# Kernel optimization log

Hardware: AMD Instinct MI355X
Metric: run time of the kernel (lower is better)

## Reference

```python
import jax, jax.numpy as jnp
import numpy as np

HEADS = 8
LATENT_LEN = 64
SEQ_LEN = 8192
DIM = 512
DIM_HEAD = DIM // HEADS
LN_EPS = 1e-5


def setup_inputs() -> dict:
    key = jax.random.key(0)
    k1, k2, k3 = jax.random.split(key, 3)
    b, n = 16, SEQ_LEN + LATENT_LEN
    x = jax.random.normal(k1, (b, n, DIM), dtype=jnp.float32)
    # torch nn.Linear weights are [out_features, in_features]
    wq = jax.random.normal(k2, (DIM, DIM), dtype=jnp.float32) * (DIM ** -0.5)
    wkv = jax.random.normal(k3, (DIM, DIM), dtype=jnp.float32) * (DIM ** -0.5)
    ln_g = jnp.ones((DIM_HEAD,), dtype=jnp.float32)
    ln_b = jnp.zeros((DIM_HEAD,), dtype=jnp.float32)
    return {"x": x, "wq": wq, "wkv": wkv, "ln_g": ln_g, "ln_b": ln_b}


def _rotate_half(t):
    # lucidrains-style rotate_half: split last dim in two halves, (-x2, x1)
    d2 = t.shape[-1] // 2
    t1, t2 = t[..., :d2], t[..., d2:]
    return jnp.concatenate([-t2, t1], axis=-1)


def _rotary_emb(n, d, dtype):
    inv_freq = 1.0 / (10000.0 ** (jnp.arange(0, d, 2, dtype=jnp.float32) / d))
    freqs = jnp.arange(n, dtype=jnp.float32)[:, None] * inv_freq[None, :]  # [n, d/2]
    emb = jnp.concatenate([freqs, freqs], axis=-1)  # [n, d]
    return jnp.cos(emb).astype(dtype), jnp.sin(emb).astype(dtype)


def reference(x, wq, wkv, ln_g, ln_b):
    b, n, dim = x.shape
    h, d = HEADS, DIM_HEAD
    context_len = n - LATENT_LEN
    scale = d ** -0.5

    q = x @ wq.T   # [b, n, dim]
    kv = x @ wkv.T # [b, n, dim]
    # rearrange 'b n (h d) -> (b h) n d'
    to_bh = lambda t: t.reshape(b, n, h, d).transpose(0, 2, 1, 3).reshape(b * h, n, d)
    q, kv = to_bh(q), to_bh(kv)

    cos, sin = _rotary_emb(n, d, x.dtype)  # [n, d] broadcast over (b h)
    rope = lambda t: t * cos + _rotate_half(t) * sin
    q, kv = rope(q), rope(kv)

    q = q * scale
    q_latent = q[:, context_len:, :]  # [(b h), latent, d]

    # LayerNorm over head dim applied to V (kv)
    mu = jnp.mean(kv, axis=-1, keepdims=True)
    var = jnp.mean(jnp.square(kv - mu), axis=-1, keepdims=True)
    lkv = (kv - mu) * jax.lax.rsqrt(var + LN_EPS) * ln_g + ln_b

    sim = jnp.einsum('bid,bjd->bij', q_latent, kv)  # [(b h), latent, n]
    attn = jax.nn.softmax(sim, axis=-1)
    out = jnp.einsum('bij,bjd->bid', attn, lkv)     # [(b h), latent, d]

    # rearrange '(b h) n d -> b n (h d)'
    out = out.reshape(b, h, LATENT_LEN, d).transpose(0, 2, 1, 3).reshape(b, LATENT_LEN, dim)
    return out
```

## Files before the change

kernel.cpp:

```cpp
#include <hip/hip_runtime.h>
#include <hip/hip_bf16.h>
#include <math.h>

#define SEQ_LEN 8192
#define LAT 64
#define NPOS 8256
#define NBATCH 16
#define NHEADS 8
#define DH 64
#define DIM 512
#define NBH 128
#define NROWS 132096
#define NCHUNK 4
#define NTILES 129

typedef unsigned short u16;
typedef unsigned int   u32;
using short8 = __attribute__((ext_vector_type(8))) short;
using f32x4  = __attribute__((ext_vector_type(4))) float;

static __device__ __forceinline__ float bf2f(u16 u) {
  union { u32 i; float f; } v; v.i = ((u32)u) << 16; return v.f;
}
static __device__ __forceinline__ u16 f2bf(float f) {
  union { float f; u32 i; } v; v.f = f;
  u32 x = v.i;
  return (u16)((x + 0x7fffu + ((x >> 16) & 1u)) >> 16);
}
static __device__ __forceinline__ void gload_lds16(const void* g, void* l) {
  __builtin_amdgcn_global_load_lds(
      (const __attribute__((address_space(1))) unsigned int*)g,
      (__attribute__((address_space(3))) unsigned int*)l, 16, 0, 0);
}

__global__ void k_rtable(float* __restrict__ ctab, float* __restrict__ stab) {
  int idx = blockIdx.x * 256 + threadIdx.x;
  int pos = idx >> 5, i = idx & 31;
  float inv = (float)(1.0 / pow(10000.0, (double)(2 * i) / 64.0));
  float ang = (float)pos * inv;
  ctab[idx] = cosf(ang);
  stab[idx] = sinf(ang);
}

__global__ __launch_bounds__(256) void k_wcast(const float* __restrict__ wkv, u16* __restrict__ wbf) {
  size_t i = (size_t)blockIdx.x * 256 + threadIdx.x;
  const float4* src = (const float4*)wkv;
  float4 a = src[2 * i], b = src[2 * i + 1];
  uint4 o;
  o.x = (u32)f2bf(a.x) | ((u32)f2bf(a.y) << 16);
  o.y = (u32)f2bf(a.z) | ((u32)f2bf(a.w) << 16);
  o.z = (u32)f2bf(b.x) | ((u32)f2bf(b.y) << 16);
  o.w = (u32)f2bf(b.z) | ((u32)f2bf(b.w) << 16);
  ((uint4*)wbf)[i] = o;
}

__global__ __launch_bounds__(256) void k_qproj(
    const float* __restrict__ x, const float* __restrict__ wq,
    const float* __restrict__ ctab, const float* __restrict__ stab,
    u16* __restrict__ qws) {
  __shared__ __align__(16) float xs[8 * 512];
  int t = threadIdx.x;
  int lr0 = blockIdx.x * 8;
  int batch = lr0 >> 6;
  int lat0 = lr0 & 63;
  for (int u = 0; u < 4; ++u) {
    int e = u * 256 + t;
    int row = e >> 7, c4 = e & 127;
    size_t m = (size_t)batch * NPOS + SEQ_LEN + lat0 + row;
    ((float4*)xs)[e] = ((const float4*)(x + m * DIM))[c4];
  }
  __syncthreads();
  float acc0[8], acc1[8];
#pragma unroll
  for (int r = 0; r < 8; ++r) { acc0[r] = 0.f; acc1[r] = 0.f; }
  const float4* w0 = (const float4*)(wq + (size_t)t * DIM);
  const float4* w1 = (const float4*)(wq + (size_t)(t + 256) * DIM);
  for (int kk = 0; kk < 128; ++kk) {
    float4 a = w0[kk], b = w1[kk];
#pragma unroll
    for (int r = 0; r < 8; ++r) {
      float4 xv = ((const float4*)xs)[r * 128 + kk];
      acc0[r] = fmaf(a.x, xv.x, fmaf(a.y, xv.y, fmaf(a.z, xv.z, fmaf(a.w, xv.w, acc0[r]))));
      acc1[r] = fmaf(b.x, xv.x, fmaf(b.y, xv.y, fmaf(b.z, xv.z, fmaf(b.w, xv.w, acc1[r]))));
    }
  }
  __syncthreads();
#pragma unroll
  for (int r = 0; r < 8; ++r) { xs[r * 512 + t] = acc0[r]; xs[r * 512 + t + 256] = acc1[r]; }
  __syncthreads();
  int rh = t >> 2, sub = t & 3;
  int row = rh >> 3, head = rh & 7;
  int lat = lat0 + row, pos = SEQ_LEN + lat;
  int bh = batch * 8 + head;
  u16* qd = qws + ((size_t)bh * LAT + lat) * DH;
#pragma unroll
  for (int u = 0; u < 8; ++u) {
    int i = sub * 8 + u;
    float v1 = xs[row * 512 + head * 64 + i];
    float v2 = xs[row * 512 + head * 64 + i + 32];
    float cc = ctab[pos * 32 + i], ss = stab[pos * 32 + i];
    qd[i]      = f2bf((v1 * cc - v2 * ss) * 0.125f);
    qd[i + 32] = f2bf((v2 * cc + v1 * ss) * 0.125f);
  }
}

__global__ __launch_bounds__(256, 2) void k_kvgemm(
    const float* __restrict__ x, const u16* __restrict__ wbf,
    const float* __restrict__ ctab, const float* __restrict__ stab,
    u16* __restrict__ kvws, float2* __restrict__ stats) {
  __shared__ __align__(16) char smem[65536];
  float* Cs = (float*)smem;
  int t = threadIdx.x;
  int lane = t & 63, w = t >> 6;
  int wr = w >> 1, wc = w & 1;
  int c = lane & 15, g = lane >> 4;
  int s = (blockIdx.x & 7) * 516 + (blockIdx.x >> 3);
  int n0 = (s & 3) * 128;
  size_t m0 = (size_t)(s >> 2) * 128;

  f32x4 acc[4][4];
#pragma unroll
  for (int mt = 0; mt < 4; ++mt)
#pragma unroll
    for (int nt = 0; nt < 4; ++nt) acc[mt][nt] = (f32x4){0.f, 0.f, 0.f, 0.f};

  int ar = t >> 3, ac8 = t & 7;
  const float* axbase = x + (m0 + ar) * DIM + ac8 * 8;
  int aswz = (ac8 * 16) ^ ((ar & 7) << 4);
  int tcs = ((t & 7) ^ (ar & 7)) << 4;
  const char* bgsrc = (const char*)(wbf + (size_t)(n0 + ar) * DIM) + tcs;

  float4 a0[4], a1[4];
  auto issueA = [&](int kt) {
#pragma unroll
    for (int u = 0; u < 4; ++u) {
      const float* p = axbase + (size_t)u * 32 * DIM + kt * 64;
      a0[u] = *(const float4*)p;
      a1[u] = *(const float4*)(p + 4);
    }
  };
  auto issueB = [&](int kt, char* bbuf) {
    const char* bg = bgsrc + kt * 128;
    char* bl = bbuf + t * 16;
#pragma unroll
    for (int u = 0; u < 4; ++u) gload_lds16(bg + (size_t)u * 32 * 1024, bl + u * 4096);
  };
  auto writeA = [&](char* abuf) {
#pragma unroll
    for (int u = 0; u < 4; ++u) {
      short8 o;
      o[0] = (short)f2bf(a0[u].x); o[1] = (short)f2bf(a0[u].y);
      o[2] = (short)f2bf(a0[u].z); o[3] = (short)f2bf(a0[u].w);
      o[4] = (short)f2bf(a1[u].x); o[5] = (short)f2bf(a1[u].y);
      o[6] = (short)f2bf(a1[u].z); o[7] = (short)f2bf(a1[u].w);
      *(short8*)(abuf + (u * 32 + ar) * 128 + aswz) = o;
    }
  };

  issueA(0);
  issueB(0, smem + 32768);
  writeA(smem);
  __syncthreads();

#pragma unroll
  for (int kt = 0; kt < 8; ++kt) {
    char* Acur = smem + (kt & 1) * 16384;
    char* Bcur = smem + 32768 + (kt & 1) * 16384;
    char* Anxt = smem + ((kt & 1) ^ 1) * 16384;
    char* Bnxt = smem + 32768 + ((kt & 1) ^ 1) * 16384;
    if (kt < 7) { issueA(kt + 1); issueB(kt + 1, Bnxt); }
#pragma unroll
    for (int ks = 0; ks < 2; ++ks) {
      short8 am[4], bn[4];
#pragma unroll
      for (int mt = 0; mt < 4; ++mt) {
        int row = wr * 64 + mt * 16 + c;
        am[mt] = *(const short8*)(Acur + row * 128 + ((ks * 64 + g * 16) ^ ((row & 7) << 4)));
      }
#pragma unroll
      for (int nt = 0; nt < 4; ++nt) {
        int row = wc * 64 + nt * 16 + c;
        bn[nt] = *(const short8*)(Bcur + row * 128 + ((ks * 64 + g * 16) ^ ((row & 7) << 4)));
      }
#pragma unroll
      for (int mt = 0; mt < 4; ++mt)
#pragma unroll
        for (int nt = 0; nt < 4; ++nt)
          acc[mt][nt] = __builtin_amdgcn_mfma_f32_16x16x32_bf16(am[mt], bn[nt], acc[mt][nt], 0, 0, 0);
    }
    if (kt < 7) writeA(Anxt);
    __syncthreads();
  }

  for (int p = 0; p < 2; ++p) {
    __syncthreads();
    if (wr == p) {
#pragma unroll
      for (int mt = 0; mt < 4; ++mt)
#pragma unroll
        for (int nt = 0; nt < 4; ++nt)
#pragma unroll
          for (int r = 0; r < 4; ++r)
            Cs[(mt * 16 + 4 * g + r) * 132 + wc * 64 + nt * 16 + c] = acc[mt][nt][r];
    }
    __syncthreads();
    if (t < 128) {
      int r_ = t & 63, hh = t >> 6;
      float v[64];
      const float4* crow = (const float4*)(Cs + r_ * 132 + hh * 64);
#pragma unroll
      for (int q = 0; q < 16; ++q) {
        float4 f = crow[q];
        v[4 * q] = f.x; v[4 * q + 1] = f.y; v[4 * q + 2] = f.z; v[4 * q + 3] = f.w;
      }
      int mi = (int)(m0 + p * 64 + r_);
      int b = mi / NPOS, pos = mi % NPOS;
      const float* ct = ctab + pos * 32;
      const float* st = stab + pos * 32;
#pragma unroll
      for (int i = 0; i < 32; ++i) {
        float cc = ct[i], ss = st[i];
        float v1 = v[i], v2 = v[i + 32];
        v[i]      = v1 * cc - v2 * ss;
        v[i + 32] = v2 * cc + v1 * ss;
      }
      float sum = 0.f;
#pragma unroll
      for (int e = 0; e < 64; ++e) sum += v[e];
      float mu = sum * 0.015625f;
      float sq = 0.f;
#pragma unroll
      for (int e = 0; e < 64; ++e) { float d = v[e] - mu; sq = fmaf(d, d, sq); }
      float rstd = rsqrtf(sq * 0.015625f + 1e-5f);
      int head = (n0 >> 6) + hh;
      int bh = b * 8 + head;
      u32 pk[32];
#pragma unroll
      for (int e = 0; e < 32; ++e) pk[e] = (u32)f2bf(v[2 * e]) | ((u32)f2bf(v[2 * e + 1]) << 16);
      uint4* dst = (uint4*)(kvws + ((size_t)bh * NPOS + pos) * DH);
#pragma unroll
      for (int u = 0; u < 8; ++u) dst[u] = make_uint4(pk[4 * u], pk[4 * u + 1], pk[4 * u + 2], pk[4 * u + 3]);
      stats[(size_t)bh * NPOS + pos] = make_float2(mu, rstd);
    }
  }
}

__global__ __launch_bounds__(256) void k_attn(
    const u16* __restrict__ qws, const u16* __restrict__ kvws,
    const float2* __restrict__ stats, const float* __restrict__ lng, const float* __restrict__ lnb,
    float* __restrict__ pout, float* __restrict__ pml) {
  __shared__ __align__(16) u16 LT[64 * 64];
  __shared__ __align__(16) u16 Pl[4][16 * 64];
  __shared__ float gl[64], bl[64];
  int t = threadIdx.x;
  int lane = t & 63, w = t >> 6;
  int c = lane & 15, g = lane >> 4;
  int bh = blockIdx.y, chunk = blockIdx.x;
  int tt0 = chunk * 33;
  int tt1 = tt0 + 33; if (tt1 > NTILES) tt1 = NTILES;
  if (t < 64) { gl[t] = lng[t]; bl[t] = lnb[t]; }
  short8 qa[2];
  {
    const u16* qrow = qws + ((size_t)bh * LAT + w * 16 + c) * DH;
    qa[0] = *(const short8*)(qrow + 8 * g);
    qa[1] = *(const short8*)(qrow + 32 + 8 * g);
  }
  f32x4 oacc[4];
#pragma unroll
  for (int nt = 0; nt < 4; ++nt) oacc[nt] = (f32x4){0.f, 0.f, 0.f, 0.f};
  float m_run[4], l_run[4];
#pragma unroll
  for (int r = 0; r < 4; ++r) { m_run[r] = -INFINITY; l_run[r] = 0.f; }
  int sj = t & 63, sw = t >> 6;
  for (int tt = tt0; tt < tt1; ++tt) {
    int j0 = tt * 64;
    __syncthreads();
    {
      const u16* src = kvws + ((size_t)bh * NPOS + j0 + sj) * DH + 16 * sw;
      short8 v0 = *(const short8*)src;
      short8 v1 = *(const short8*)(src + 8);
      float2 stv = stats[(size_t)bh * NPOS + j0 + sj];
      float A = stv.y, C = -stv.x * stv.y;
      char* ltb = (char*)LT;
#pragma unroll
      for (int e = 0; e < 16; ++e) {
        int dd = 16 * sw + e;
        u16 uv = (u16)((e < 8) ? v0[e] : v1[e - 8]);
        float y = fmaf(bf2f(uv), A, C);
        y = fmaf(y, gl[dd], bl[dd]);
        *(u16*)(ltb + dd * 128 + ((2 * sj) ^ ((dd & 7) << 4))) = f2bf(y);
      }
    }
    __syncthreads();
    f32x4 sacc[4];
#pragma unroll
    for (int jn = 0; jn < 4; ++jn) sacc[jn] = (f32x4){0.f, 0.f, 0.f, 0.f};
    const u16* kb = kvws + ((size_t)bh * NPOS + j0) * DH;
#pragma unroll
    for (int ks = 0; ks < 2; ++ks)
#pragma unroll
      for (int jn = 0; jn < 4; ++jn) {
        short8 kf = *(const short8*)(kb + (size_t)(jn * 16 + c) * DH + ks * 32 + 8 * g);
        sacc[jn] = __builtin_amdgcn_mfma_f32_16x16x32_bf16(qa[ks], kf, sacc[jn], 0, 0, 0);
      }
    char* pb = (char*)Pl[w];
#pragma unroll
    for (int r = 0; r < 4; ++r) {
      float mt0 = fmaxf(fmaxf(sacc[0][r], sacc[1][r]), fmaxf(sacc[2][r], sacc[3][r]));
      mt0 = fmaxf(mt0, __shfl_xor(mt0, 1));
      mt0 = fmaxf(mt0, __shfl_xor(mt0, 2));
      mt0 = fmaxf(mt0, __shfl_xor(mt0, 4));
      mt0 = fmaxf(mt0, __shfl_xor(mt0, 8));
      float mnew = fmaxf(m_run[r], mt0);
      float corr = __expf(m_run[r] - mnew);
      m_run[r] = mnew;
      float ts = 0.f;
#pragma unroll
      for (int jn = 0; jn < 4; ++jn) {
        float p = __expf(sacc[jn][r] - mnew);
        sacc[jn][r] = p;
        ts += p;
      }
      ts += __shfl_xor(ts, 1); ts += __shfl_xor(ts, 2);
      ts += __shfl_xor(ts, 4); ts += __shfl_xor(ts, 8);
      l_run[r] = l_run[r] * corr + ts;
#pragma unroll
      for (int nt = 0; nt < 4; ++nt) oacc[nt][r] *= corr;
      int i = 4 * g + r;
      int isw = (i & 7) << 4;
#pragma unroll
      for (int jn = 0; jn < 4; ++jn) {
        int j = jn * 16 + c;
        *(u16*)(pb + i * 128 + ((2 * j) ^ isw)) = f2bf(sacc[jn][r]);
      }
    }
#pragma unroll
    for (int ks = 0; ks < 2; ++ks) {
      short8 pa = *(const short8*)(pb + c * 128 + ((ks * 64 + 16 * g) ^ ((c & 7) << 4)));
#pragma unroll
      for (int nt = 0; nt < 4; ++nt) {
        int dd = nt * 16 + c;
        short8 lv = *(const short8*)((char*)LT + dd * 128 + ((ks * 64 + 16 * g) ^ ((dd & 7) << 4)));
        oacc[nt] = __builtin_amdgcn_mfma_f32_16x16x32_bf16(pa, lv, oacc[nt], 0, 0, 0);
      }
    }
  }
  size_t ob = (size_t)bh * NCHUNK + chunk;
#pragma unroll
  for (int nt = 0; nt < 4; ++nt)
#pragma unroll
    for (int r = 0; r < 4; ++r) {
      int i = w * 16 + 4 * g + r;
      pout[(ob * 64 + i) * 64 + nt * 16 + c] = oacc[nt][r];
    }
  if (c == 0) {
#pragma unroll
    for (int r = 0; r < 4; ++r) {
      int i = w * 16 + 4 * g + r;
      pml[(ob * 2 + 0) * 64 + i] = m_run[r];
      pml[(ob * 2 + 1) * 64 + i] = l_run[r];
    }
  }
}

__global__ __launch_bounds__(256) void k_combine(
    const float* __restrict__ pout, const float* __restrict__ pml, float* __restrict__ out) {
  int bh = blockIdx.x, t = threadIdx.x;
  int i = t >> 2, dq = t & 3;
  float mv[NCHUNK], lv[NCHUNK];
#pragma unroll
  for (int cc = 0; cc < NCHUNK; ++cc) {
    size_t ob = (size_t)bh * NCHUNK + cc;
    mv[cc] = pml[(ob * 2 + 0) * 64 + i];
    lv[cc] = pml[(ob * 2 + 1) * 64 + i];
  }
  float M = fmaxf(fmaxf(mv[0], mv[1]), fmaxf(mv[2], mv[3]));
  float wsum = 0.f, wcf[NCHUNK];
#pragma unroll
  for (int cc = 0; cc < NCHUNK; ++cc) { wcf[cc] = __expf(mv[cc] - M); wsum = fmaf(wcf[cc], lv[cc], wsum); }
  float inv = 1.0f / wsum;
#pragma unroll
  for (int e = 0; e < 16; ++e) {
    int dd = dq * 16 + e;
    float a = 0.f;
#pragma unroll
    for (int cc = 0; cc < NCHUNK; ++cc)
      a = fmaf(wcf[cc], pout[(((size_t)bh * NCHUNK + cc) * 64 + i) * 64 + dd], a);
    out[((size_t)(bh >> 3) * LAT + i) * DIM + (bh & 7) * DH + dd] = a * inv;
  }
}

extern "C" void kernel_launch(void* const* d_in, const int* in_sizes, int n_in,
                              void* d_out, int out_size, void* d_ws, size_t ws_size,
                              hipStream_t stream) {
  const float* x   = (const float*)d_in[0];
  const float* wq  = (const float*)d_in[1];
  const float* wkv = (const float*)d_in[2];
  const float* lng = (const float*)d_in[3];
  const float* lnb = (const float*)d_in[4];
  float* out = (float*)d_out;
  char* ws = (char*)d_ws;
  size_t off = 0;
  auto alloc = [&](size_t bytes) { char* p = ws + off; off += (bytes + 255) & ~(size_t)255; return p; };
  float*  ctab  = (float*)alloc((size_t)NPOS * 32 * 4);
  float*  stab  = (float*)alloc((size_t)NPOS * 32 * 4);
  u16*    qws   = (u16*)alloc((size_t)NBH * LAT * DH * 2);
  u16*    kvws  = (u16*)alloc((size_t)NBH * NPOS * DH * 2);
  float2* stats = (float2*)alloc((size_t)NBH * NPOS * 8);
  float*  pout  = (float*)alloc((size_t)NBH * NCHUNK * 64 * 64 * 4);
  float*  pml   = (float*)alloc((size_t)NBH * NCHUNK * 2 * 64 * 4);
  u16*    wbf   = (u16*)alloc((size_t)DIM * DIM * 2);
  (void)in_sizes; (void)n_in; (void)out_size; (void)ws_size;

  hipLaunchKernelGGL(k_rtable, dim3(NPOS * 32 / 256), dim3(256), 0, stream, ctab, stab);
  hipLaunchKernelGGL(k_wcast, dim3(DIM * DIM / 8 / 256), dim3(256), 0, stream, wkv, wbf);
  hipLaunchKernelGGL(k_qproj, dim3(128), dim3(256), 0, stream, x, wq, ctab, stab, qws);
  hipLaunchKernelGGL(k_kvgemm, dim3(4128), dim3(256), 0, stream, x, wbf, ctab, stab, kvws, stats);
  hipLaunchKernelGGL(k_attn, dim3(NCHUNK, NBH), dim3(256), 0, stream, qws, kvws, stats, lng, lnb, pout, pml);
  hipLaunchKernelGGL(k_combine, dim3(NBH), dim3(256), 0, stream, pout, pml, out);
}
```

Before: 393.5 us.

## Fold LayerNorm of V into softmax weights and double attention split-K chunks

The attention kernel no longer normalizes each V tile in shared memory. It scales the probabilities by each key's rstd, accumulates a running sum of p*mu*rstd, and applies gamma, beta and the mean correction in the combine step. This removes per-element LayerNorm arithmetic and the gamma/beta shared-memory lookups from the inner loop. The number of KV chunks per head also goes from 4 to 8, doubling the grid from 512 to 1024 blocks for better occupancy, at the cost of more partial outputs to write and combine. Precision changes slightly because V is now fed raw in bf16 and P*rstd is rounded to bf16.

```diff
diff --git a/kernel.cpp b/kernel.cpp
--- a/kernel.cpp
+++ b/kernel.cpp
@@ -11,8 +11,9 @@
 #define DIM 512
 #define NBH 128
 #define NROWS 132096
-#define NCHUNK 4
+#define NCHUNK 8
 #define NTILES 129
+#define TPC 17
 
 typedef unsigned short u16;
 typedef unsigned int   u32;
@@ -247,18 +248,16 @@
 
 __global__ __launch_bounds__(256) void k_attn(
     const u16* __restrict__ qws, const u16* __restrict__ kvws,
-    const float2* __restrict__ stats, const float* __restrict__ lng, const float* __restrict__ lnb,
+    const float2* __restrict__ stats,
     float* __restrict__ pout, float* __restrict__ pml) {
   __shared__ __align__(16) u16 LT[64 * 64];
   __shared__ __align__(16) u16 Pl[4][16 * 64];
-  __shared__ float gl[64], bl[64];
   int t = threadIdx.x;
   int lane = t & 63, w = t >> 6;
   int c = lane & 15, g = lane >> 4;
   int bh = blockIdx.y, chunk = blockIdx.x;
-  int tt0 = chunk * 33;
-  int tt1 = tt0 + 33; if (tt1 > NTILES) tt1 = NTILES;
-  if (t < 64) { gl[t] = lng[t]; bl[t] = lnb[t]; }
+  int tt0 = chunk * TPC;
+  int tt1 = tt0 + TPC; if (tt1 > NTILES) tt1 = NTILES;
   short8 qa[2];
   {
     const u16* qrow = qws + ((size_t)bh * LAT + w * 16 + c) * DH;
@@ -268,9 +267,9 @@
   f32x4 oacc[4];
 #pragma unroll
   for (int nt = 0; nt < 4; ++nt) oacc[nt] = (f32x4){0.f, 0.f, 0.f, 0.f};
-  float m_run[4], l_run[4];
-#pragma unroll
-  for (int r = 0; r < 4; ++r) { m_run[r] = -INFINITY; l_run[r] = 0.f; }
+  float m_run[4], l_run[4], q2_run[4];
+#pragma unroll
+  for (int r = 0; r < 4; ++r) { m_run[r] = -INFINITY; l_run[r] = 0.f; q2_run[r] = 0.f; }
   int sj = t & 63, sw = t >> 6;
   for (int tt = tt0; tt < tt1; ++tt) {
     int j0 = tt * 64;
@@ -279,16 +278,12 @@
       const u16* src = kvws + ((size_t)bh * NPOS + j0 + sj) * DH + 16 * sw;
       short8 v0 = *(const short8*)src;
       short8 v1 = *(const short8*)(src + 8);
-      float2 stv = stats[(size_t)bh * NPOS + j0 + sj];
-      float A = stv.y, C = -stv.x * stv.y;
       char* ltb = (char*)LT;
 #pragma unroll
       for (int e = 0; e < 16; ++e) {
         int dd = 16 * sw + e;
         u16 uv = (u16)((e < 8) ? v0[e] : v1[e - 8]);
-        float y = fmaf(bf2f(uv), A, C);
-        y = fmaf(y, gl[dd], bl[dd]);
-        *(u16*)(ltb + dd * 128 + ((2 * sj) ^ ((dd & 7) << 4))) = f2bf(y);
+        *(u16*)(ltb + dd * 128 + ((2 * sj) ^ ((dd & 7) << 4))) = uv;
       }
     }
     __syncthreads();
@@ -303,6 +298,12 @@
         short8 kf = *(const short8*)(kb + (size_t)(jn * 16 + c) * DH + ks * 32 + 8 * g);
         sacc[jn] = __builtin_amdgcn_mfma_f32_16x16x32_bf16(qa[ks], kf, sacc[jn], 0, 0, 0);
       }
+    float rsd[4], musig[4];
+#pragma unroll
+    for (int jn = 0; jn < 4; ++jn) {
+      float2 sv = stats[(size_t)bh * NPOS + j0 + jn * 16 + c];
+      rsd[jn] = sv.y; musig[jn] = sv.x * sv.y;
+    }
     char* pb = (char*)Pl[w];
 #pragma unroll
     for (int r = 0; r < 4; ++r) {
@@ -314,16 +315,20 @@
       float mnew = fmaxf(m_run[r], mt0);
       float corr = __expf(m_run[r] - mnew);
       m_run[r] = mnew;
-      float ts = 0.f;
+      float ts = 0.f, tq = 0.f;
 #pragma unroll
       for (int jn = 0; jn < 4; ++jn) {
         float p = __expf(sacc[jn][r] - mnew);
-        sacc[jn][r] = p;
         ts += p;
+        tq = fmaf(p, musig[jn], tq);
+        sacc[jn][r] = p * rsd[jn];
       }
       ts += __shfl_xor(ts, 1); ts += __shfl_xor(ts, 2);
       ts += __shfl_xor(ts, 4); ts += __shfl_xor(ts, 8);
-      l_run[r] = l_run[r] * corr + ts;
+      tq += __shfl_xor(tq, 1); tq += __shfl_xor(tq, 2);
+      tq += __shfl_xor(tq, 4); tq += __shfl_xor(tq, 8);
+      l_run[r]  = l_run[r]  * corr + ts;
+      q2_run[r] = q2_run[r] * corr + tq;
 #pragma unroll
       for (int nt = 0; nt < 4; ++nt) oacc[nt][r] *= corr;
       int i = 4 * g + r;
@@ -357,36 +362,47 @@
 #pragma unroll
     for (int r = 0; r < 4; ++r) {
       int i = w * 16 + 4 * g + r;
-      pml[(ob * 2 + 0) * 64 + i] = m_run[r];
-      pml[(ob * 2 + 1) * 64 + i] = l_run[r];
+      pml[(ob * 3 + 0) * 64 + i] = m_run[r];
+      pml[(ob * 3 + 1) * 64 + i] = l_run[r];
+      pml[(ob * 3 + 2) * 64 + i] = q2_run[r];
     }
   }
 }
 
 __global__ __launch_bounds__(256) void k_combine(
-    const float* __restrict__ pout, const float* __restrict__ pml, float* __restrict__ out) {
+    const float* __restrict__ pout, const float* __restrict__ pml,
+    const float* __restrict__ lng, const float* __restrict__ lnb,
+    float* __restrict__ out) {
   int bh = blockIdx.x, t = threadIdx.x;
   int i = t >> 2, dq = t & 3;
-  float mv[NCHUNK], lv[NCHUNK];
+  float mv[NCHUNK], lv[NCHUNK], qv[NCHUNK];
 #pragma unroll
   for (int cc = 0; cc < NCHUNK; ++cc) {
     size_t ob = (size_t)bh * NCHUNK + cc;
-    mv[cc] = pml[(ob * 2 + 0) * 64 + i];
-    lv[cc] = pml[(ob * 2 + 1) * 64 + i];
-  }
-  float M = fmaxf(fmaxf(mv[0], mv[1]), fmaxf(mv[2], mv[3]));
-  float wsum = 0.f, wcf[NCHUNK];
-#pragma unroll
-  for (int cc = 0; cc < NCHUNK; ++cc) { wcf[cc] = __expf(mv[cc] - M); wsum = fmaf(wcf[cc], lv[cc], wsum); }
-  float inv = 1.0f / wsum;
+    mv[cc] = pml[(ob * 3 + 0) * 64 + i];
+    lv[cc] = pml[(ob * 3 + 1) * 64 + i];
+    qv[cc] = pml[(ob * 3 + 2) * 64 + i];
+  }
+  float M = -INFINITY;
+#pragma unroll
+  for (int cc = 0; cc < NCHUNK; ++cc) M = fmaxf(M, mv[cc]);
+  float L = 0.f, Q2 = 0.f, wcf[NCHUNK];
+#pragma unroll
+  for (int cc = 0; cc < NCHUNK; ++cc) {
+    wcf[cc] = __expf(mv[cc] - M);
+    L = fmaf(wcf[cc], lv[cc], L);
+    Q2 = fmaf(wcf[cc], qv[cc], Q2);
+  }
+  float invL = 1.0f / L;
 #pragma unroll
   for (int e = 0; e < 16; ++e) {
     int dd = dq * 16 + e;
-    float a = 0.f;
+    float O = 0.f;
 #pragma unroll
     for (int cc = 0; cc < NCHUNK; ++cc)
-      a = fmaf(wcf[cc], pout[(((size_t)bh * NCHUNK + cc) * 64 + i) * 64 + dd], a);
-    out[((size_t)(bh >> 3) * LAT + i) * DIM + (bh & 7) * DH + dd] = a * inv;
+      O = fmaf(wcf[cc], pout[(((size_t)bh * NCHUNK + cc) * 64 + i) * 64 + dd], O);
+    float val = (lng[dd] * (O - Q2) + lnb[dd] * L) * invL;
+    out[((size_t)(bh >> 3) * LAT + i) * DIM + (bh & 7) * DH + dd] = val;
   }
 }
 
@@ -408,7 +424,7 @@
   u16*    kvws  = (u16*)alloc((size_t)NBH * NPOS * DH * 2);
   float2* stats = (float2*)alloc((size_t)NBH * NPOS * 8);
   float*  pout  = (float*)alloc((size_t)NBH * NCHUNK * 64 * 64 * 4);
-  float*  pml   = (float*)alloc((size_t)NBH * NCHUNK * 2 * 64 * 4);
+  float*  pml   = (float*)alloc((size_t)NBH * NCHUNK * 3 * 64 * 4);
   u16*    wbf   = (u16*)alloc((size_t)DIM * DIM * 2);
   (void)in_sizes; (void)n_in; (void)out_size; (void)ws_size;
 
@@ -416,6 +432,6 @@
   hipLaunchKernelGGL(k_wcast, dim3(DIM * DIM / 8 / 256), dim3(256), 0, stream, wkv, wbf);
   hipLaunchKernelGGL(k_qproj, dim3(128), dim3(256), 0, stream, x, wq, ctab, stab, qws);
   hipLaunchKernelGGL(k_kvgemm, dim3(4128), dim3(256), 0, stream, x, wbf, ctab, stab, kvws, stats);
-  hipLaunchKernelGGL(k_attn, dim3(NCHUNK, NBH), dim3(256), 0, stream, qws, kvws, stats, lng, lnb, pout, pml);
-  hipLaunchKernelGGL(k_combine, dim3(NBH), dim3(256), 0, stream, pout, pml, out);
-}
+  hipLaunchKernelGGL(k_attn, dim3(NCHUNK, NBH), dim3(256), 0, stream, qws, kvws, stats, pout, pml);
+  hipLaunchKernelGGL(k_combine, dim3(NBH), dim3(256), 0, stream, pout, pml, lng, lnb, out);
+}
```

Result: slower. 412.1 us (+4.7%).
